# Performance work log

Measured on AMD Instinct MI355X. Metric: run time of the kernel, lower is better.

Reference implementation:

```python
import jax, jax.numpy as jnp
import numpy as np

LN_EPS = 1e-5

def _conv2d(x, w, b, pad):
    # x: [B,C,H,W], w: [O,I,kh,kw] -> [B,O,H,W]
    y = jax.lax.conv_general_dilated(
        x, w, window_strides=(1, 1), padding=[(pad, pad), (pad, pad)],
        dimension_numbers=('NCHW', 'OIHW', 'NCHW'))
    return y + b[None, :, None, None]

def setup_inputs() -> dict:
    key = jax.random.key(0)
    ks = jax.random.split(key, 12)
    B, C, H, W = 4, 256, 64, 64
    D = 64  # inner_projection
    s_in = 1.0 / np.sqrt(C)
    s_d1 = 1.0 / np.sqrt(D)
    s_d3 = 1.0 / np.sqrt(D * 9)
    return {
        'x':     jax.random.normal(ks[0], (B, C, H, W), jnp.float32),
        'w_in':  jax.random.normal(ks[1], (D, C, 1, 1), jnp.float32) * s_in,
        'b_in':  jnp.zeros((D,), jnp.float32),
        'wq':    jax.random.normal(ks[2], (D, D, 3, 3), jnp.float32) * s_d3,
        'bq':    jnp.zeros((D,), jnp.float32),
        'wk':    jax.random.normal(ks[3], (D, D, 3, 3), jnp.float32) * s_d3,
        'bk':    jnp.zeros((D,), jnp.float32),
        'wv':    jax.random.normal(ks[4], (D, D, 3, 3), jnp.float32) * s_d3,
        'bv':    jnp.zeros((D,), jnp.float32),
        'w_out': jax.random.normal(ks[5], (C, D, 1, 1), jnp.float32) * s_d1,
        'b_out': jnp.zeros((C,), jnp.float32),
        'gamma': jax.random.normal(ks[6], (1,), jnp.float32) * 0.1,
        'ln_w':  jnp.ones((C,), jnp.float32),
        'ln_b':  jnp.zeros((C,), jnp.float32),
    }

def _attention(q, k, v):
    # full-pixel attention, NO 1/sqrt(d) scale (matches source)
    B, C, H, W = v.shape
    N = H * W
    qf = q.reshape(B, -1, N)   # [B,d,N]
    kf = k.reshape(B, -1, N)
    vf = v.reshape(B, -1, N)
    energy = jnp.einsum('bci,bcj->bij', qf, kf)      # [B,N,N] = Q^T K
    attn = jax.nn.softmax(energy, axis=-1)
    out = jnp.einsum('bcj,bij->bci', vf, attn)        # V @ attn^T
    return out.reshape(B, C, H, W)

def _layernorm2d(x, w, b):
    # normalize over channel dim per pixel (LayerNorm2d)
    mu = jnp.mean(x, axis=1, keepdims=True)
    var = jnp.var(x, axis=1, keepdims=True)
    xn = (x - mu) * jax.lax.rsqrt(var + LN_EPS)
    return xn * w[None, :, None, None] + b[None, :, None, None]

def reference(x, w_in, b_in, wq, bq, wk, bk, wv, bv, w_out, b_out, gamma, ln_w, ln_b):
    att = _conv2d(x, w_in, b_in, 0)          # inner projection [B,D,H,W]
    q = _conv2d(att, wq, bq, 1)
    k = _conv2d(att, wk, bk, 1)
    v = _conv2d(att, wv, bv, 1)
    att = _attention(q, k, v)
    att = _conv2d(att, w_out, b_out, 0)       # outer projection [B,C,H,W]
    return _layernorm2d(gamma * x + att, ln_w, ln_b)
```

## Files before the change

### kernel.cpp

```cpp
#include <hip/hip_runtime.h>
#include <hip/hip_bf16.h>

#define BB 4
#define CC 256
#define DD 64
#define HH 64
#define WW 64
#define NN 4096
#define NSPLIT 4
#define VST 68
#define SM_SHIFT2 92.332482616893664f
#define LOG2E 1.4426950408889634f

typedef __hip_bfloat16 bf16;
typedef __attribute__((ext_vector_type(8))) short bf16x8;
typedef __attribute__((ext_vector_type(4))) float f32x4;
typedef __attribute__((ext_vector_type(4))) short s16x4;

#define MFMA16(a, b, c) __builtin_amdgcn_mfma_f32_16x16x32_bf16(a, b, c, 0, 0, 0)

#if __has_builtin(__builtin_amdgcn_mfma_f32_16x16x16bf16_1k)
static __device__ __forceinline__ f32x4 MFMA16K(s16x4 a, s16x4 b, f32x4 c) {
  return __builtin_amdgcn_mfma_f32_16x16x16bf16_1k(a, b, c, 0, 0, 0);
}
#else
static __device__ __forceinline__ f32x4 MFMA16K(s16x4 a, s16x4 b, f32x4 c) {
  f32x4 d;
  asm("v_mfma_f32_16x16x16_bf16 %0, %1, %2, %3"
      : "=&v"(d) : "v"(a), "v"(b), "v"(c));
  return d;
}
#endif

#if __has_builtin(__builtin_amdgcn_exp2f)
#define EXP2F(x) __builtin_amdgcn_exp2f(x)
#else
#define EXP2F(x) exp2f(x)
#endif

static __device__ __forceinline__ float ldin(const void* p, size_t i, bool isb) {
  return isb ? __bfloat162float(((const bf16*)p)[i]) : ((const float*)p)[i];
}
static __device__ __forceinline__ void stout(void* p, size_t i, float v, bool isb) {
  if (isb) ((bf16*)p)[i] = __float2bfloat16(v);
  else     ((float*)p)[i] = v;
}
static __device__ __forceinline__ unsigned pack2(bf16 a, bf16 b) {
  unsigned short ua = *reinterpret_cast<unsigned short*>(&a);
  unsigned short ub = *reinterpret_cast<unsigned short*>(&b);
  return (unsigned)ua | ((unsigned)ub << 16);
}
static __device__ __forceinline__ bool probe_bf16(const unsigned* lnw) {
  return lnw[0] == 0x3F803F80u;
}

__global__ __launch_bounds__(256) void k_wt(
    const void* __restrict__ wq, const void* __restrict__ wk,
    const void* __restrict__ wv, const void* __restrict__ w_in,
    const void* __restrict__ w_out,
    bf16* __restrict__ Wth, bf16* __restrict__ Wtl,
    bf16* __restrict__ Win_h, bf16* __restrict__ Win_l,
    bf16* __restrict__ Wo_h, bf16* __restrict__ Wo_l,
    const unsigned* __restrict__ lnw) {
  const bool isb = probe_bf16(lnw);
  int u = blockIdx.x * 256 + threadIdx.x;
  if (u < 110592) {
    int c3 = u / 36864, rem = u % 36864;
    int tap = rem / 4096, r2 = rem % 4096;
    int oc = r2 >> 6, ic = r2 & 63;
    const void* w = (c3 == 0) ? wq : ((c3 == 1) ? wk : wv);
    float v = ldin(w, (size_t)oc * 576 + ic * 9 + tap, isb);
    bf16 h = __float2bfloat16(v);
    Wth[u] = h;
    Wtl[u] = __float2bfloat16(v - __bfloat162float(h));
  } else if (u < 126976) {
    int v2 = u - 110592;
    float v = ldin(w_in, v2, isb);
    bf16 h = __float2bfloat16(v);
    Win_h[v2] = h;
    Win_l[v2] = __float2bfloat16(v - __bfloat162float(h));
  } else {
    int v2 = u - 126976;
    float v = ldin(w_out, v2, isb);
    bf16 h = __float2bfloat16(v);
    Wo_h[v2] = h;
    Wo_l[v2] = __float2bfloat16(v - __bfloat162float(h));
  }
}

__global__ __launch_bounds__(256) void k_conv_in(
    const void* __restrict__ x,
    const bf16* __restrict__ Win_h, const bf16* __restrict__ Win_l,
    const void* __restrict__ bias, bf16* __restrict__ att_h,
    bf16* __restrict__ att_l, const unsigned* __restrict__ lnw) {
  __shared__ __align__(16) short Xh[32 * 64];
  __shared__ __align__(16) short Xl[32 * 64];
  const bool isb = probe_bf16(lnw);
  const int b = blockIdx.y, n0 = blockIdx.x * 32;
  const int t = threadIdx.x;
  const int w = t >> 6, lane = t & 63, quad = lane >> 4, l16 = lane & 15;
  const int l7 = l16 & 7;
  const size_t xoff = (size_t)b * CC * NN;
  const int sdd = t >> 3, sn4 = (t & 7) * 4;
  f32x4 acc[2];
  #pragma unroll
  for (int nt = 0; nt < 2; ++nt)
    #pragma unroll
    for (int r = 0; r < 4; ++r)
      acc[nt][r] = ldin(bias, w * 16 + quad * 4 + r, isb);
  for (int c0 = 0; c0 < CC; c0 += 64) {
    __syncthreads();
    {
      float a0[4], a1[4];
      size_t i0a = xoff + (size_t)(c0 + 2 * sdd) * NN + n0 + sn4;
      if (!isb) {
        const float* xp = (const float*)x;
        float4 va = *(const float4*)&xp[i0a];
        float4 vb = *(const float4*)&xp[i0a + NN];
        a0[0] = va.x; a0[1] = va.y; a0[2] = va.z; a0[3] = va.w;
        a1[0] = vb.x; a1[1] = vb.y; a1[2] = vb.z; a1[3] = vb.w;
      } else {
        #pragma unroll
        for (int j = 0; j < 4; ++j) {
          a0[j] = ldin(x, i0a + j, true);
          a1[j] = ldin(x, i0a + NN + j, true);
        }
      }
      #pragma unroll
      for (int j = 0; j < 4; ++j) {
        int n = sn4 + j;
        bf16 h0 = __float2bfloat16(a0[j]), h1 = __float2bfloat16(a1[j]);
        bf16 l0 = __float2bfloat16(a0[j] - __bfloat162float(h0));
        bf16 l1 = __float2bfloat16(a1[j] - __bfloat162float(h1));
        int cs = ((sdd >> 2) ^ (n & 7)) * 8 + ((2 * sdd) & 7);
        *(unsigned*)&Xh[n * 64 + cs] = pack2(h0, h1);
        *(unsigned*)&Xl[n * 64 + cs] = pack2(l0, l1);
      }
    }
    __syncthreads();
    #pragma unroll
    for (int kc = 0; kc < 2; ++kc) {
      size_t woff = (size_t)(w * 16 + l16) * 256 + c0 + kc * 32 + quad * 8;
      bf16x8 wh = *(const bf16x8*)(Win_h + woff);
      bf16x8 wl = *(const bf16x8*)(Win_l + woff);
      const int xo = ((kc * 4 + quad) ^ l7) * 8;
      #pragma unroll
      for (int nt = 0; nt < 2; ++nt) {
        int rn = nt * 16 + l16;
        bf16x8 xh = *(const bf16x8*)&Xh[rn * 64 + xo];
        bf16x8 xl = *(const bf16x8*)&Xl[rn * 64 + xo];
        acc[nt] = MFMA16(wh, xh, acc[nt]);
        acc[nt] = MFMA16(wh, xl, acc[nt]);
        acc[nt] = MFMA16(wl, xh, acc[nt]);
      }
    }
  }
  #pragma unroll
  for (int nt = 0; nt < 2; ++nt) {
    size_t off = ((size_t)b * NN + n0 + nt * 16 + l16) * DD + w * 16 + quad * 4;
    bf16 h[4], l[4];
    #pragma unroll
    for (int r = 0; r < 4; ++r) {
      float v = acc[nt][r];
      h[r] = __float2bfloat16(v);
      l[r] = __float2bfloat16(v - __bfloat162float(h[r]));
    }
    *(uint2*)&att_h[off] = make_uint2(pack2(h[0], h[1]), pack2(h[2], h[3]));
    *(uint2*)&att_l[off] = make_uint2(pack2(l[0], l[1]), pack2(l[2], l[3]));
  }
}

__global__ __launch_bounds__(256) void k_conv3(
    const bf16* __restrict__ att_h, const bf16* __restrict__ att_l,
    const bf16* __restrict__ Wth, const bf16* __restrict__ Wtl,
    const void* __restrict__ bq, const void* __restrict__ bk,
    const void* __restrict__ bv,
    bf16* __restrict__ qth, bf16* __restrict__ qtl,
    bf16* __restrict__ kth, bf16* __restrict__ ktl,
    bf16* __restrict__ vt, const unsigned* __restrict__ lnw) {
  __shared__ __align__(16) short Ah[3 * 66 * 64];
  __shared__ __align__(16) short Al[3 * 66 * 64];
  float* o_s = reinterpret_cast<float*>(Ah);
  const bool isb = probe_bf16(lnw);
  const int y = blockIdx.x, b = blockIdx.y, c3 = blockIdx.z;
  const int t = threadIdx.x;
  const int w = t >> 6, lane = t & 63, quad = lane >> 4, l16 = lane & 15;
  const uint4 z4 = make_uint4(0, 0, 0, 0);
  #pragma unroll
  for (int r = 0; r < 3; ++r) {
    int yp = y + r - 1;
    bool ok = (unsigned)yp < 64u;
    const uint4* sh = (const uint4*)(att_h + ((size_t)b * NN + (size_t)yp * 64) * DD);
    const uint4* sl = (const uint4*)(att_l + ((size_t)b * NN + (size_t)yp * 64) * DD);
    #pragma unroll
    for (int ii = 0; ii < 2; ++ii) {
      int u = t + ii * 256;
      int xx = u >> 3, ch = u & 7;
      int rr = r * 66 + xx + 1;
      uint4 vh = ok ? sh[u] : z4;
      uint4 vl = ok ? sl[u] : z4;
      int cs = (ch ^ (rr & 7)) * 8;
      *(uint4*)&Ah[rr * 64 + cs] = vh;
      *(uint4*)&Al[rr * 64 + cs] = vl;
    }
    if (t < 16) {
      int rr = r * 66 + ((t & 1) ? 65 : 0);
      int cs = (t >> 1) * 8;
      *(uint4*)&Ah[rr * 64 + cs] = z4;
      *(uint4*)&Al[rr * 64 + cs] = z4;
    }
  }
  __syncthreads();
  const void* bp = (c3 == 0) ? bq : ((c3 == 1) ? bk : bv);
  const bf16* wth = Wth + (size_t)c3 * 9 * 4096;
  const bf16* wtl = Wtl + (size_t)c3 * 9 * 4096;
  f32x4 acc[4];
  #pragma unroll
  for (int nt = 0; nt < 4; ++nt)
    #pragma unroll
    for (int r = 0; r < 4; ++r)
      acc[nt][r] = ldin(bp, w * 16 + quad * 4 + r, isb);
  #pragma unroll
  for (int tap = 0; tap < 9; ++tap) {
    const int dy = tap / 3, dx = tap % 3;
    const int woff = tap * 4096 + (w * 16 + l16) * 64 + quad * 8;
    bf16x8 wh0 = *(const bf16x8*)(wth + woff);
    bf16x8 wh1 = *(const bf16x8*)(wth + woff + 32);
    bf16x8 wl0 = *(const bf16x8*)(wtl + woff);
    bf16x8 wl1 = *(const bf16x8*)(wtl + woff + 32);
    #pragma unroll
    for (int nt = 0; nt < 4; ++nt) {
      int rr = dy * 66 + nt * 16 + l16 + dx;
      int chA = (quad ^ (rr & 7)) * 8;
      int chB = ((quad + 4) ^ (rr & 7)) * 8;
      bf16x8 ah0 = *(const bf16x8*)&Ah[rr * 64 + chA];
      bf16x8 ah1 = *(const bf16x8*)&Ah[rr * 64 + chB];
      bf16x8 al0 = *(const bf16x8*)&Al[rr * 64 + chA];
      bf16x8 al1 = *(const bf16x8*)&Al[rr * 64 + chB];
      acc[nt] = MFMA16(wh0, ah0, acc[nt]);
      acc[nt] = MFMA16(wh1, ah1, acc[nt]);
      acc[nt] = MFMA16(wh0, al0, acc[nt]);
      acc[nt] = MFMA16(wh1, al1, acc[nt]);
      acc[nt] = MFMA16(wl0, ah0, acc[nt]);
      acc[nt] = MFMA16(wl1, ah1, acc[nt]);
    }
  }
  if (c3 < 2) {
    bf16* dh = (c3 == 0) ? qth : kth;
    bf16* dl = (c3 == 0) ? qtl : ktl;
    const float qsc = (c3 == 0) ? LOG2E : 1.0f;
    const size_t rowb = (size_t)b * NN + (size_t)y * 64;
    #pragma unroll
    for (int nt = 0; nt < 4; ++nt) {
      size_t off = (rowb + nt * 16 + l16) * DD + w * 16 + quad * 4;
      bf16 h[4], l[4];
      #pragma unroll
      for (int r = 0; r < 4; ++r) {
        float v = acc[nt][r] * qsc;
        h[r] = __float2bfloat16(v);
        l[r] = __float2bfloat16(v - __bfloat162float(h[r]));
      }
      *(uint2*)&dh[off] = make_uint2(pack2(h[0], h[1]), pack2(h[2], h[3]));
      *(uint2*)&dl[off] = make_uint2(pack2(l[0], l[1]), pack2(l[2], l[3]));
    }
  } else {
    __syncthreads();
    #pragma unroll
    for (int nt = 0; nt < 4; ++nt)
      #pragma unroll
      for (int r = 0; r < 4; ++r)
        o_s[(nt * 16 + l16) * 65 + w * 16 + quad * 4 + r] = acc[nt][r];
    __syncthreads();
    #pragma unroll
    for (int i = 0; i < 8; ++i) {
      int u = t + i * 256;
      int c = u >> 5, np = (u & 31) * 2;
      float v0 = o_s[np * 65 + c], v1 = o_s[(np + 1) * 65 + c];
      *(unsigned*)&vt[((size_t)b * DD + c) * NN + (size_t)y * 64 + np] =
          pack2(__float2bfloat16(v0), __float2bfloat16(v1));
    }
  }
}

__global__ __launch_bounds__(256) void k_attn(
    const bf16* __restrict__ qth, const bf16* __restrict__ qtl,
    const bf16* __restrict__ kth, const bf16* __restrict__ ktl,
    const bf16* __restrict__ vt, float* __restrict__ po,
    float* __restrict__ pl) {
  __shared__ __align__(16) short Kh[2][64 * 64];
  __shared__ __align__(16) short Kl[2][64 * 64];
  __shared__ __align__(16) short Vs[2][64 * VST];
  const int b = blockIdx.y, i0 = blockIdx.x * 128, sp = blockIdx.z;
  const int jt0 = sp * (64 / NSPLIT), jt1 = jt0 + (64 / NSPLIT);
  const int t = threadIdx.x;
  const int w = t >> 6, lane = t & 63, quad = lane >> 4, l16 = lane & 15;
  const int l7 = l16 & 7;
  const int xA = (quad ^ l7) * 8;
  const int xB = ((quad + 4) ^ l7) * 8;
  const int sr = t >> 2, m4 = t & 3, sg = m4 * 16;
  const int sc0 = ((2 * m4) ^ (sr & 7)) * 8;
  const int sc1 = ((2 * m4 + 1) ^ (sr & 7)) * 8;
  bf16x8 qf_h0[2], qf_h1[2], qf_l0[2], qf_l1[2];
  #pragma unroll
  for (int is = 0; is < 2; ++is) {
    size_t qoff = ((size_t)b * NN + i0 + is * 64 + w * 16 + l16) * DD + quad * 8;
    qf_h0[is] = *(const bf16x8*)(qth + qoff);
    qf_h1[is] = *(const bf16x8*)(qth + qoff + 32);
    qf_l0[is] = *(const bf16x8*)(qtl + qoff);
    qf_l1[is] = *(const bf16x8*)(qtl + qoff + 32);
  }
  uint4 kh0, kh1, kl0, kl1, vx0, vx1;
  {
    size_t koff = ((size_t)b * NN + jt0 * 64 + sr) * DD + sg;
    kh0 = ((const uint4*)(kth + koff))[0]; kh1 = ((const uint4*)(kth + koff))[1];
    kl0 = ((const uint4*)(ktl + koff))[0]; kl1 = ((const uint4*)(ktl + koff))[1];
    size_t voff = ((size_t)b * DD + sr) * NN + jt0 * 64 + sg;
    vx0 = ((const uint4*)(vt + voff))[0];  vx1 = ((const uint4*)(vt + voff))[1];
  }
  *(uint4*)&Kh[0][sr * 64 + sc0] = kh0;   *(uint4*)&Kh[0][sr * 64 + sc1] = kh1;
  *(uint4*)&Kl[0][sr * 64 + sc0] = kl0;   *(uint4*)&Kl[0][sr * 64 + sc1] = kl1;
  *(uint4*)&Vs[0][sr * VST + sc0] = vx0;  *(uint4*)&Vs[0][sr * VST + sc1] = vx1;
  __syncthreads();
  s16x4 onesf;
  onesf[0] = onesf[1] = onesf[2] = onesf[3] = (short)0x3F80;
  f32x4 lacc[2] = {};
  f32x4 oacc[4][2] = {};
  int p = 0;
  for (int jt = jt0; jt < jt1; ++jt) {
    const bool more = (jt < jt1 - 1);
    if (more) {
      int j0n = (jt + 1) * 64;
      size_t koff = ((size_t)b * NN + j0n + sr) * DD + sg;
      kh0 = ((const uint4*)(kth + koff))[0]; kh1 = ((const uint4*)(kth + koff))[1];
      kl0 = ((const uint4*)(ktl + koff))[0]; kl1 = ((const uint4*)(ktl + koff))[1];
      size_t voff = ((size_t)b * DD + sr) * NN + j0n + sg;
      vx0 = ((const uint4*)(vt + voff))[0];  vx1 = ((const uint4*)(vt + voff))[1];
    }
    const short* khp = Kh[p];
    const short* klp = Kl[p];
    const short* vsp = Vs[p];
    s16x4 pf[2][4];
    __builtin_amdgcn_s_setprio(1);
    #pragma unroll
    for (int mt = 0; mt < 4; ++mt) {
      int r0 = (mt * 16 + l16) * 64;
      bf16x8 kf_h0 = *(const bf16x8*)&khp[r0 + xA];
      bf16x8 kf_h1 = *(const bf16x8*)&khp[r0 + xB];
      bf16x8 kf_l0 = *(const bf16x8*)&klp[r0 + xA];
      bf16x8 kf_l1 = *(const bf16x8*)&klp[r0 + xB];
      #pragma unroll
      for (int is = 0; is < 2; ++is) {
        f32x4 c = {0.f, 0.f, 0.f, 0.f};
        c = MFMA16(kf_h0, qf_h0[is], c);
        c = MFMA16(kf_h1, qf_h1[is], c);
        c = MFMA16(kf_h0, qf_l0[is], c);
        c = MFMA16(kf_h1, qf_l1[is], c);
        c = MFMA16(kf_l0, qf_h0[is], c);
        c = MFMA16(kf_l1, qf_h1[is], c);
        s16x4 pk;
        #pragma unroll
        for (int r = 0; r < 4; ++r) {
          float pexp = EXP2F(c[r] - SM_SHIFT2);
          bf16 ph = __float2bfloat16(pexp);
          pk[r] = *reinterpret_cast<short*>(&ph);
        }
        pf[is][mt] = pk;
      }
    }
    __builtin_amdgcn_s_setprio(0);
    if (more) {
      short* khn = Kh[p ^ 1];
      short* kln = Kl[p ^ 1];
      *(uint4*)&khn[sr * 64 + sc0] = kh0;  *(uint4*)&khn[sr * 64 + sc1] = kh1;
      *(uint4*)&kln[sr * 64 + sc0] = kl0;  *(uint4*)&kln[sr * 64 + sc1] = kl1;
    }
    __builtin_amdgcn_s_setprio(1);
    #pragma unroll
    for (int mt = 0; mt < 4; ++mt) {
      int rv = (mt * 16 + l16) * VST;
      #pragma unroll
      for (int kt = 0; kt < 4; ++kt) {
        s16x4 vf = *(const s16x4*)
            &vsp[rv + ((kt * 2 + (quad >> 1)) ^ l7) * 8 + (quad & 1) * 4];
        oacc[mt][0] = MFMA16K(vf, pf[0][kt], oacc[mt][0]);
        oacc[mt][1] = MFMA16K(vf, pf[1][kt], oacc[mt][1]);
      }
    }
    #pragma unroll
    for (int kt = 0; kt < 4; ++kt) {
      lacc[0] = MFMA16K(onesf, pf[0][kt], lacc[0]);
      lacc[1] = MFMA16K(onesf, pf[1][kt], lacc[1]);
    }
    __builtin_amdgcn_s_setprio(0);
    if (more) {
      short* vsn = Vs[p ^ 1];
      *(uint4*)&vsn[sr * VST + sc0] = vx0; *(uint4*)&vsn[sr * VST + sc1] = vx1;
    }
    __syncthreads();
    p ^= 1;
  }
  const size_t SEGC = (size_t)BB * DD * NN;
  #pragma unroll
  for (int is = 0; is < 2; ++is) {
    const int ig = i0 + is * 64 + w * 16 + l16;
    #pragma unroll
    for (int mt = 0; mt < 4; ++mt)
      #pragma unroll
      for (int r = 0; r < 4; ++r) {
        int c = mt * 16 + quad * 4 + r;
        po[(size_t)sp * SEGC + ((size_t)b * DD + c) * NN + ig] = oacc[mt][is][r];
      }
    if (quad == 0) pl[((size_t)sp * BB + b) * NN + ig] = lacc[is][0];
  }
}

__global__ __launch_bounds__(256) void k_out_ln(
    const float* __restrict__ po, const float* __restrict__ pl,
    const void* __restrict__ x,
    const bf16* __restrict__ Wo_h, const bf16* __restrict__ Wo_l,
    const void* __restrict__ bias, const void* __restrict__ gamma,
    const void* __restrict__ lw, const void* __restrict__ lb,
    void* __restrict__ out, const unsigned* __restrict__ lnw) {
  __shared__ __align__(16) short Ahs[32 * 64];
  __shared__ __align__(16) short Als[32 * 64];
  __shared__ __align__(16) float Obuf[256 * 36];
  __shared__ float inv_s[32];
  __shared__ float red1[32 * 4], red2[32 * 4];
  __shared__ float mu_s[32], rs_s[32];
  __shared__ float lw_s[256], lb_s[256];
  const bool isb = probe_bf16(lnw);
  const int b = blockIdx.y, n0 = blockIdx.x * 32;
  const int t = threadIdx.x;
  const int w = t >> 6, lane = t & 63, quad = lane >> 4, l16 = lane & 15;
  const int l7 = l16 & 7;
  const size_t SEGC = (size_t)BB * DD * NN;
  if (t < 32) {
    int i = n0 + t;
    float lsum = 0.f;
    #pragma unroll
    for (int s = 0; s < NSPLIT; ++s) lsum += pl[((size_t)s * BB + b) * NN + i];
    inv_s[t] = 1.f / lsum;
  }
  lw_s[t] = ldin(lw, t, isb);
  lb_s[t] = ldin(lb, t, isb);
  const float g = ldin(gamma, 0, isb);
  __syncthreads();
  {
    const int dd = t >> 3, n4 = (t & 7) * 4;
    size_t base = ((size_t)b * DD + 2 * dd) * NN + n0 + n4;
    float v0[4] = {0.f, 0.f, 0.f, 0.f}, v1[4] = {0.f, 0.f, 0.f, 0.f};
    #pragma unroll
    for (int s = 0; s < NSPLIT; ++s) {
      float4 pa = *(const float4*)&po[(size_t)s * SEGC + base];
      float4 pb = *(const float4*)&po[(size_t)s * SEGC + base + NN];
      v0[0] += pa.x; v0[1] += pa.y; v0[2] += pa.z; v0[3] += pa.w;
      v1[0] += pb.x; v1[1] += pb.y; v1[2] += pb.z; v1[3] += pb.w;
    }
    #pragma unroll
    for (int j = 0; j < 4; ++j) {
      int n = n4 + j;
      float inv = inv_s[n];
      float a0 = v0[j] * inv, a1 = v1[j] * inv;
      bf16 h0 = __float2bfloat16(a0), h1 = __float2bfloat16(a1);
      bf16 l0 = __float2bfloat16(a0 - __bfloat162float(h0));
      bf16 l1 = __float2bfloat16(a1 - __bfloat162float(h1));
      int cs = ((dd >> 2) ^ (n & 7)) * 8 + ((2 * dd) & 7);
      *(unsigned*)&Ahs[n * 64 + cs] = pack2(h0, h1);
      *(unsigned*)&Als[n * 64 + cs] = pack2(l0, l1);
    }
  }
  f32x4 acc[4][2];
  #pragma unroll
  for (int oct = 0; oct < 4; ++oct)
    #pragma unroll
    for (int r = 0; r < 4; ++r) {
      float bo = ldin(bias, w * 64 + oct * 16 + quad * 4 + r, isb);
      #pragma unroll
      for (int nt = 0; nt < 2; ++nt) acc[oct][nt][r] = bo;
    }
  __syncthreads();
  #pragma unroll
  for (int oct = 0; oct < 4; ++oct) {
    const int base = w * 64 + oct * 16;
    #pragma unroll
    for (int kc = 0; kc < 2; ++kc) {
      size_t woff = (size_t)(base + l16) * 64 + kc * 32 + quad * 8;
      bf16x8 wh = *(const bf16x8*)(Wo_h + woff);
      bf16x8 wl = *(const bf16x8*)(Wo_l + woff);
      const int xo = ((kc * 4 + quad) ^ l7) * 8;
      #pragma unroll
      for (int nt = 0; nt < 2; ++nt) {
        int rn = nt * 16 + l16;
        bf16x8 ah = *(const bf16x8*)&Ahs[rn * 64 + xo];
        bf16x8 al = *(const bf16x8*)&Als[rn * 64 + xo];
        acc[oct][nt] = MFMA16(wh, ah, acc[oct][nt]);
        acc[oct][nt] = MFMA16(wh, al, acc[oct][nt]);
        acc[oct][nt] = MFMA16(wl, ah, acc[oct][nt]);
      }
    }
  }
  #pragma unroll
  for (int nt = 0; nt < 2; ++nt) {
    int nn = nt * 16 + l16;
    float s1 = 0.f, s2 = 0.f;
    #pragma unroll
    for (int oct = 0; oct < 4; ++oct)
      #pragma unroll
      for (int r = 0; r < 4; ++r) {
        int oc = w * 64 + oct * 16 + quad * 4 + r;
        float xv = ldin(x, ((size_t)b * CC + oc) * NN + n0 + nn, isb);
        float y = acc[oct][nt][r] + g * xv;
        acc[oct][nt][r] = y;
        s1 += y; s2 += y * y;
      }
    s1 += __shfl_xor(s1, 16, 64); s1 += __shfl_xor(s1, 32, 64);
    s2 += __shfl_xor(s2, 16, 64); s2 += __shfl_xor(s2, 32, 64);
    if (quad == 0) { red1[nn * 4 + w] = s1; red2[nn * 4 + w] = s2; }
  }
  __syncthreads();
  if (t < 32) {
    float sm = red1[t * 4] + red1[t * 4 + 1] + red1[t * 4 + 2] + red1[t * 4 + 3];
    float sq = red2[t * 4] + red2[t * 4 + 1] + red2[t * 4 + 2] + red2[t * 4 + 3];
    float mu = sm * (1.f / 256.f);
    float var = sq * (1.f / 256.f) - mu * mu;
    mu_s[t] = mu;
    rs_s[t] = rsqrtf(var + 1e-5f);
  }
  __syncthreads();
  if (!isb) {
    #pragma unroll
    for (int nt = 0; nt < 2; ++nt) {
      int nn = nt * 16 + l16;
      float mu = mu_s[nn], rs = rs_s[nn];
      #pragma unroll
      for (int oct = 0; oct < 4; ++oct)
        #pragma unroll
        for (int r = 0; r < 4; ++r) {
          int oc = w * 64 + oct * 16 + quad * 4 + r;
          Obuf[oc * 36 + nn] = (acc[oct][nt][r] - mu) * rs * lw_s[oc] + lb_s[oc];
        }
    }
    __syncthreads();
    const int oc8 = t >> 3, pxq = (t & 7) * 4;
    float* op = (float*)out + (size_t)b * CC * NN + n0 + pxq;
    #pragma unroll
    for (int p2 = 0; p2 < 8; ++p2) {
      int oc = p2 * 32 + oc8;
      float4 v = *(const float4*)&Obuf[oc * 36 + pxq];
      *(float4*)&op[(size_t)oc * NN] = v;
    }
  } else {
    #pragma unroll
    for (int nt = 0; nt < 2; ++nt) {
      int nn = nt * 16 + l16;
      float mu = mu_s[nn], rs = rs_s[nn];
      #pragma unroll
      for (int oct = 0; oct < 4; ++oct)
        #pragma unroll
        for (int r = 0; r < 4; ++r) {
          int oc = w * 64 + oct * 16 + quad * 4 + r;
          float o = (acc[oct][nt][r] - mu) * rs * lw_s[oc] + lb_s[oc];
          stout(out, ((size_t)b * CC + oc) * NN + n0 + nn, o, isb);
        }
    }
  }
}

extern "C" void kernel_launch(void* const* d_in, const int* in_sizes, int n_in,
                              void* d_out, int out_size, void* d_ws, size_t ws_size,
                              hipStream_t stream) {
  const void* x     = d_in[0];
  const void* w_in  = d_in[1];
  const void* b_in  = d_in[2];
  const void* wq    = d_in[3];
  const void* bq    = d_in[4];
  const void* wk    = d_in[5];
  const void* bk    = d_in[6];
  const void* wv    = d_in[7];
  const void* bv    = d_in[8];
  const void* w_out = d_in[9];
  const void* b_out = d_in[10];
  const void* gamma = d_in[11];
  const void* ln_w  = d_in[12];
  const void* ln_b  = d_in[13];

  const size_t SEG = (size_t)BB * DD * NN;
  char*  p     = (char*)d_ws;
  bf16*  att_h = (bf16*)p;  p += SEG * 2;
  bf16*  att_l = (bf16*)p;  p += SEG * 2;
  bf16*  qth   = (bf16*)p;  p += SEG * 2;
  bf16*  qtl   = (bf16*)p;  p += SEG * 2;
  bf16*  kth   = (bf16*)p;  p += SEG * 2;
  bf16*  ktl   = (bf16*)p;  p += SEG * 2;
  bf16*  vt    = (bf16*)p;  p += SEG * 2;
  float* po    = (float*)p; p += (size_t)NSPLIT * SEG * 4;
  float* pl    = (float*)p; p += (size_t)NSPLIT * BB * NN * 4;
  bf16*  Wth   = (bf16*)p;  p += 110592 * 2;
  bf16*  Wtl   = (bf16*)p;  p += 110592 * 2;
  bf16*  Win_h = (bf16*)p;  p += 16384 * 2;
  bf16*  Win_l = (bf16*)p;  p += 16384 * 2;
  bf16*  Wo_h  = (bf16*)p;  p += 16384 * 2;
  bf16*  Wo_l  = (bf16*)p;  p += 16384 * 2;
  const unsigned* lnw = (const unsigned*)ln_w;

  k_wt<<<560, 256, 0, stream>>>(wq, wk, wv, w_in, w_out, Wth, Wtl,
                                Win_h, Win_l, Wo_h, Wo_l, lnw);
  k_conv_in<<<dim3(NN / 32, BB), 256, 0, stream>>>(x, Win_h, Win_l, b_in,
                                                   att_h, att_l, lnw);
  k_conv3<<<dim3(64, BB, 3), 256, 0, stream>>>(att_h, att_l, Wth, Wtl,
                                               bq, bk, bv,
                                               qth, qtl, kth, ktl, vt, lnw);
  k_attn<<<dim3(NN / 128, BB, NSPLIT), 256, 0, stream>>>(qth, qtl, kth, ktl, vt,
                                                         po, pl);
  k_out_ln<<<dim3(NN / 32, BB), 256, 0, stream>>>(po, pl, x, Wo_h, Wo_l,
                                                  b_out, gamma, ln_w, ln_b,
                                                  d_out, lnw);
}
```

Baseline: 174.8 us.

## Software-pipeline attention: overlap QK^T/exp of next tile with PV of previous

Restructures the attention inner loop so the QK^T MFMAs and exp for tile j are interleaved with the PV and row-sum MFMAs for tile j-1, using a prologue and epilogue. V gets a triple-buffered LDS ring so the previous tile's V stays valid while the next one is written. Global prefetch now runs two tiles ahead and there is a single barrier per iteration. The aim is to hide exp/VALU latency behind MFMA work, at the cost of more registers for the extra P tile and more LDS.

```diff
diff --git a/kernel.cpp b/kernel.cpp
--- a/kernel.cpp
+++ b/kernel.cpp
@@ -289,7 +289,7 @@
     float* __restrict__ pl) {
   __shared__ __align__(16) short Kh[2][64 * 64];
   __shared__ __align__(16) short Kl[2][64 * 64];
-  __shared__ __align__(16) short Vs[2][64 * VST];
+  __shared__ __align__(16) short Vs[3][64 * VST];
   const int b = blockIdx.y, i0 = blockIdx.x * 128, sp = blockIdx.z;
   const int jt0 = sp * (64 / NSPLIT), jt1 = jt0 + (64 / NSPLIT);
   const int t = threadIdx.x;
@@ -309,37 +309,33 @@
     qf_l0[is] = *(const bf16x8*)(qtl + qoff);
     qf_l1[is] = *(const bf16x8*)(qtl + qoff + 32);
   }
+  const bf16* khg = kth + ((size_t)b * NN + jt0 * 64 + sr) * DD + sg;
+  const bf16* klg = ktl + ((size_t)b * NN + jt0 * 64 + sr) * DD + sg;
+  const bf16* vg  = vt  + ((size_t)b * DD + sr) * NN + jt0 * 64 + sg;
   uint4 kh0, kh1, kl0, kl1, vx0, vx1;
-  {
-    size_t koff = ((size_t)b * NN + jt0 * 64 + sr) * DD + sg;
-    kh0 = ((const uint4*)(kth + koff))[0]; kh1 = ((const uint4*)(kth + koff))[1];
-    kl0 = ((const uint4*)(ktl + koff))[0]; kl1 = ((const uint4*)(ktl + koff))[1];
-    size_t voff = ((size_t)b * DD + sr) * NN + jt0 * 64 + sg;
-    vx0 = ((const uint4*)(vt + voff))[0];  vx1 = ((const uint4*)(vt + voff))[1];
-  }
-  *(uint4*)&Kh[0][sr * 64 + sc0] = kh0;   *(uint4*)&Kh[0][sr * 64 + sc1] = kh1;
-  *(uint4*)&Kl[0][sr * 64 + sc0] = kl0;   *(uint4*)&Kl[0][sr * 64 + sc1] = kl1;
-  *(uint4*)&Vs[0][sr * VST + sc0] = vx0;  *(uint4*)&Vs[0][sr * VST + sc1] = vx1;
+  const int s0 = jt0 % 3;
+  kh0 = ((const uint4*)khg)[0]; kh1 = ((const uint4*)khg)[1];
+  kl0 = ((const uint4*)klg)[0]; kl1 = ((const uint4*)klg)[1];
+  vx0 = ((const uint4*)vg)[0];  vx1 = ((const uint4*)vg)[1];
+  khg += 64 * DD; klg += 64 * DD; vg += 64;
+  *(uint4*)&Kh[0][sr * 64 + sc0] = kh0;    *(uint4*)&Kh[0][sr * 64 + sc1] = kh1;
+  *(uint4*)&Kl[0][sr * 64 + sc0] = kl0;    *(uint4*)&Kl[0][sr * 64 + sc1] = kl1;
+  *(uint4*)&Vs[s0][sr * VST + sc0] = vx0;  *(uint4*)&Vs[s0][sr * VST + sc1] = vx1;
+  kh0 = ((const uint4*)khg)[0]; kh1 = ((const uint4*)khg)[1];
+  kl0 = ((const uint4*)klg)[0]; kl1 = ((const uint4*)klg)[1];
+  vx0 = ((const uint4*)vg)[0];  vx1 = ((const uint4*)vg)[1];
+  khg += 64 * DD; klg += 64 * DD; vg += 64;
   __syncthreads();
   s16x4 onesf;
   onesf[0] = onesf[1] = onesf[2] = onesf[3] = (short)0x3F80;
   f32x4 lacc[2] = {};
   f32x4 oacc[4][2] = {};
-  int p = 0;
-  for (int jt = jt0; jt < jt1; ++jt) {
-    const bool more = (jt < jt1 - 1);
-    if (more) {
-      int j0n = (jt + 1) * 64;
-      size_t koff = ((size_t)b * NN + j0n + sr) * DD + sg;
-      kh0 = ((const uint4*)(kth + koff))[0]; kh1 = ((const uint4*)(kth + koff))[1];
-      kl0 = ((const uint4*)(ktl + koff))[0]; kl1 = ((const uint4*)(ktl + koff))[1];
-      size_t voff = ((size_t)b * DD + sr) * NN + j0n + sg;
-      vx0 = ((const uint4*)(vt + voff))[0];  vx1 = ((const uint4*)(vt + voff))[1];
-    }
-    const short* khp = Kh[p];
-    const short* klp = Kl[p];
-    const short* vsp = Vs[p];
-    s16x4 pf[2][4];
+  s16x4 pfP[2][4];
+  int vw = (s0 + 1 == 3) ? 0 : s0 + 1;
+  int vr = s0;
+  {
+    const short* khp = Kh[0];
+    const short* klp = Kl[0];
     __builtin_amdgcn_s_setprio(1);
     #pragma unroll
     for (int mt = 0; mt < 4; ++mt) {
@@ -348,32 +344,99 @@
       bf16x8 kf_h1 = *(const bf16x8*)&khp[r0 + xB];
       bf16x8 kf_l0 = *(const bf16x8*)&klp[r0 + xA];
       bf16x8 kf_l1 = *(const bf16x8*)&klp[r0 + xB];
-      #pragma unroll
-      for (int is = 0; is < 2; ++is) {
-        f32x4 c = {0.f, 0.f, 0.f, 0.f};
-        c = MFMA16(kf_h0, qf_h0[is], c);
-        c = MFMA16(kf_h1, qf_h1[is], c);
-        c = MFMA16(kf_h0, qf_l0[is], c);
-        c = MFMA16(kf_h1, qf_l1[is], c);
-        c = MFMA16(kf_l0, qf_h0[is], c);
-        c = MFMA16(kf_l1, qf_h1[is], c);
-        s16x4 pk;
+      f32x4 c0 = {0.f, 0.f, 0.f, 0.f}, c1 = {0.f, 0.f, 0.f, 0.f};
+      c0 = MFMA16(kf_h0, qf_h0[0], c0);  c0 = MFMA16(kf_h1, qf_h1[0], c0);
+      c0 = MFMA16(kf_h0, qf_l0[0], c0);  c0 = MFMA16(kf_h1, qf_l1[0], c0);
+      c0 = MFMA16(kf_l0, qf_h0[0], c0);  c0 = MFMA16(kf_l1, qf_h1[0], c0);
+      c1 = MFMA16(kf_h0, qf_h0[1], c1);  c1 = MFMA16(kf_h1, qf_h1[1], c1);
+      c1 = MFMA16(kf_h0, qf_l0[1], c1);  c1 = MFMA16(kf_h1, qf_l1[1], c1);
+      c1 = MFMA16(kf_l0, qf_h0[1], c1);  c1 = MFMA16(kf_l1, qf_h1[1], c1);
+      #pragma unroll
+      for (int r = 0; r < 4; ++r) {
+        float e0 = EXP2F(c0[r] - SM_SHIFT2);
+        float e1 = EXP2F(c1[r] - SM_SHIFT2);
+        bf16 p0 = __float2bfloat16(e0), p1 = __float2bfloat16(e1);
+        pfP[0][mt][r] = *reinterpret_cast<short*>(&p0);
+        pfP[1][mt][r] = *reinterpret_cast<short*>(&p1);
+      }
+    }
+    __builtin_amdgcn_s_setprio(0);
+    *(uint4*)&Kh[1][sr * 64 + sc0] = kh0;    *(uint4*)&Kh[1][sr * 64 + sc1] = kh1;
+    *(uint4*)&Kl[1][sr * 64 + sc0] = kl0;    *(uint4*)&Kl[1][sr * 64 + sc1] = kl1;
+    *(uint4*)&Vs[vw][sr * VST + sc0] = vx0;  *(uint4*)&Vs[vw][sr * VST + sc1] = vx1;
+    vw = (vw + 1 == 3) ? 0 : vw + 1;
+    kh0 = ((const uint4*)khg)[0]; kh1 = ((const uint4*)khg)[1];
+    kl0 = ((const uint4*)klg)[0]; kl1 = ((const uint4*)klg)[1];
+    vx0 = ((const uint4*)vg)[0];  vx1 = ((const uint4*)vg)[1];
+    khg += 64 * DD; klg += 64 * DD; vg += 64;
+    __syncthreads();
+  }
+  for (int jt = jt0 + 1; jt < jt1; ++jt) {
+    const short* khp = Kh[jt & 1];
+    const short* klp = Kl[jt & 1];
+    const short* vpp = Vs[vr];
+    s16x4 pfC[2][4];
+    __builtin_amdgcn_s_setprio(1);
+    #pragma unroll
+    for (int mt = 0; mt < 4; ++mt) {
+      int r0 = (mt * 16 + l16) * 64;
+      bf16x8 kf_h0 = *(const bf16x8*)&khp[r0 + xA];
+      bf16x8 kf_h1 = *(const bf16x8*)&khp[r0 + xB];
+      bf16x8 kf_l0 = *(const bf16x8*)&klp[r0 + xA];
+      bf16x8 kf_l1 = *(const bf16x8*)&klp[r0 + xB];
+      f32x4 c0 = {0.f, 0.f, 0.f, 0.f}, c1 = {0.f, 0.f, 0.f, 0.f};
+      c0 = MFMA16(kf_h0, qf_h0[0], c0);  c0 = MFMA16(kf_h1, qf_h1[0], c0);
+      c0 = MFMA16(kf_h0, qf_l0[0], c0);  c0 = MFMA16(kf_h1, qf_l1[0], c0);
+      c0 = MFMA16(kf_l0, qf_h0[0], c0);  c0 = MFMA16(kf_l1, qf_h1[0], c0);
+      c1 = MFMA16(kf_h0, qf_h0[1], c1);  c1 = MFMA16(kf_h1, qf_h1[1], c1);
+      c1 = MFMA16(kf_h0, qf_l0[1], c1);  c1 = MFMA16(kf_h1, qf_l1[1], c1);
+      c1 = MFMA16(kf_l0, qf_h0[1], c1);  c1 = MFMA16(kf_l1, qf_h1[1], c1);
+      {
+        int rv = (mt * 16 + l16) * VST;
         #pragma unroll
-        for (int r = 0; r < 4; ++r) {
-          float pexp = EXP2F(c[r] - SM_SHIFT2);
-          bf16 ph = __float2bfloat16(pexp);
-          pk[r] = *reinterpret_cast<short*>(&ph);
+        for (int kt = 0; kt < 4; ++kt) {
+          s16x4 vf = *(const s16x4*)
+              &vpp[rv + ((kt * 2 + (quad >> 1)) ^ l7) * 8 + (quad & 1) * 4];
+          oacc[mt][0] = MFMA16K(vf, pfP[0][kt], oacc[mt][0]);
+          oacc[mt][1] = MFMA16K(vf, pfP[1][kt], oacc[mt][1]);
         }
-        pf[is][mt] = pk;
+        lacc[0] = MFMA16K(onesf, pfP[0][mt], lacc[0]);
+        lacc[1] = MFMA16K(onesf, pfP[1][mt], lacc[1]);
+      }
+      #pragma unroll
+      for (int r = 0; r < 4; ++r) {
+        float e0 = EXP2F(c0[r] - SM_SHIFT2);
+        float e1 = EXP2F(c1[r] - SM_SHIFT2);
+        bf16 p0 = __float2bfloat16(e0), p1 = __float2bfloat16(e1);
+        pfC[0][mt][r] = *reinterpret_cast<short*>(&p0);
+        pfC[1][mt][r] = *reinterpret_cast<short*>(&p1);
       }
     }
     __builtin_amdgcn_s_setprio(0);
-    if (more) {
-      short* khn = Kh[p ^ 1];
-      short* kln = Kl[p ^ 1];
+    if (jt + 1 < jt1) {
+      short* khn = Kh[(jt + 1) & 1];
+      short* kln = Kl[(jt + 1) & 1];
+      short* vsn = Vs[vw];
       *(uint4*)&khn[sr * 64 + sc0] = kh0;  *(uint4*)&khn[sr * 64 + sc1] = kh1;
       *(uint4*)&kln[sr * 64 + sc0] = kl0;  *(uint4*)&kln[sr * 64 + sc1] = kl1;
-    }
+      *(uint4*)&vsn[sr * VST + sc0] = vx0; *(uint4*)&vsn[sr * VST + sc1] = vx1;
+    }
+    vw = (vw + 1 == 3) ? 0 : vw + 1;
+    vr = (vr + 1 == 3) ? 0 : vr + 1;
+    if (jt + 2 < jt1) {
+      kh0 = ((const uint4*)khg)[0]; kh1 = ((const uint4*)khg)[1];
+      kl0 = ((const uint4*)klg)[0]; kl1 = ((const uint4*)klg)[1];
+      vx0 = ((const uint4*)vg)[0];  vx1 = ((const uint4*)vg)[1];
+      khg += 64 * DD; klg += 64 * DD; vg += 64;
+    }
+    __syncthreads();
+    #pragma unroll
+    for (int is = 0; is < 2; ++is)
+      #pragma unroll
+      for (int m2 = 0; m2 < 4; ++m2) pfP[is][m2] = pfC[is][m2];
+  }
+  {
+    const short* vpp = Vs[vr];
     __builtin_amdgcn_s_setprio(1);
     #pragma unroll
     for (int mt = 0; mt < 4; ++mt) {
@@ -381,23 +444,14 @@
       #pragma unroll
       for (int kt = 0; kt < 4; ++kt) {
         s16x4 vf = *(const s16x4*)
-            &vsp[rv + ((kt * 2 + (quad >> 1)) ^ l7) * 8 + (quad & 1) * 4];
-        oacc[mt][0] = MFMA16K(vf, pf[0][kt], oacc[mt][0]);
-        oacc[mt][1] = MFMA16K(vf, pf[1][kt], oacc[mt][1]);
-      }
-    }
-    #pragma unroll
-    for (int kt = 0; kt < 4; ++kt) {
-      lacc[0] = MFMA16K(onesf, pf[0][kt], lacc[0]);
-      lacc[1] = MFMA16K(onesf, pf[1][kt], lacc[1]);
+            &vpp[rv + ((kt * 2 + (quad >> 1)) ^ l7) * 8 + (quad & 1) * 4];
+        oacc[mt][0] = MFMA16K(vf, pfP[0][kt], oacc[mt][0]);
+        oacc[mt][1] = MFMA16K(vf, pfP[1][kt], oacc[mt][1]);
+      }
+      lacc[0] = MFMA16K(onesf, pfP[0][mt], lacc[0]);
+      lacc[1] = MFMA16K(onesf, pfP[1][mt], lacc[1]);
     }
     __builtin_amdgcn_s_setprio(0);
-    if (more) {
-      short* vsn = Vs[p ^ 1];
-      *(uint4*)&vsn[sr * VST + sc0] = vx0; *(uint4*)&vsn[sr * VST + sc1] = vx1;
-    }
-    __syncthreads();
-    p ^= 1;
   }
   const size_t SEGC = (size_t)BB * DD * NN;
   #pragma unroll
```

After: 172.8 us. No clear change (-1.1%).
